# Optimization experiments

Measured on AMD Instinct MI355X. Metric: run time of the kernel, lower is better.

Reference implementation:

```python
import jax, jax.numpy as jnp
import numpy as np

N, E, D, NHID, NOUT, G = 100000, 600000, 128, 512, 768, 2048
EPS = 1e-5

def _lin_init(k, fi, fo):
    s = 1.0 / np.sqrt(fi)
    kw, kb = jax.random.split(k)
    W = jax.random.uniform(kw, (fi, fo), jnp.float32, -s, s)
    b = jax.random.uniform(kb, (fo,), jnp.float32, -s, s)
    return W, b

def setup_inputs():
    key = jax.random.key(0)
    ks = jax.random.split(key, 16)
    inp = {}
    inp['x'] = jax.random.normal(ks[0], (N, D), jnp.float32)
    inp['edge_index'] = jax.random.randint(ks[1], (2, E), 0, N, jnp.int32)
    inp['batch'] = jnp.sort(jax.random.randint(ks[2], (N,), 0, G, jnp.int32))
    # 3 GCN layers + GAT attention layer + 4 MLP linears
    inp['W1'], inp['b1'] = _lin_init(ks[3], D, D)
    inp['W2'], inp['b2'] = _lin_init(ks[4], D, D)
    inp['W3'], inp['b3'] = _lin_init(ks[5], D, D)
    inp['Wa'], inp['ba'] = _lin_init(ks[6], D, D)
    ka1, ka2 = jax.random.split(ks[7])
    inp['a_src'] = jax.random.normal(ka1, (D,), jnp.float32) * 0.1
    inp['a_dst'] = jax.random.normal(ka2, (D,), jnp.float32) * 0.1
    # batchnorm affine params (4 BNs)
    for i, nm in enumerate(['g1', 'g2', 'g3', 'ga']):
        inp[nm] = jnp.ones((D,), jnp.float32)
        inp['be' + nm[1:]] = jnp.zeros((D,), jnp.float32)
    inp['Wl1'], inp['bl1'] = _lin_init(ks[8], D, NHID)
    inp['Wl2'], inp['bl2'] = _lin_init(ks[9], NHID, NHID)
    inp['Wl3'], inp['bl3'] = _lin_init(ks[10], NHID, NHID)
    inp['Wl4'], inp['bl4'] = _lin_init(ks[11], NHID, NOUT)
    inp['gln'] = jnp.ones((NOUT,), jnp.float32)
    inp['bln'] = jnp.zeros((NOUT,), jnp.float32)
    return inp

def _bn(x, g, b):
    # training-mode batchnorm over node dim (biased variance, like torch)
    mu = jnp.mean(x, axis=0)
    var = jnp.var(x, axis=0)
    return (x - mu) * jax.lax.rsqrt(var + EPS) * g + b

def _forward(x, edge_index, batch, W1, b1, g1, be1, W2, b2, g2, be2, W3, b3, g3, be3,
             Wa, ba, a_src, a_dst, ga, bea, Wl1, bl1, Wl2, bl2, Wl3, bl3, Wl4, bl4, gln, bln):
    loop = jnp.arange(N, dtype=edge_index.dtype)
    src = jnp.concatenate([edge_index[0], loop])  # [E+N] with self-loops
    dst = jnp.concatenate([edge_index[1], loop])
    deg = jax.ops.segment_sum(jnp.ones_like(dst, jnp.float32), dst, num_segments=N)
    dinv = jax.lax.rsqrt(deg)  # deg >= 1 thanks to self-loops
    norm = (dinv[src] * dinv[dst])[:, None]  # [E+N, 1]

    def gcn(h, W, b):
        h = h @ W
        return jax.ops.segment_sum(h[src] * norm, dst, num_segments=N) + b

    x = jax.nn.relu(_bn(gcn(x, W1, b1), g1, be1)) + x
    x = jax.nn.relu(_bn(gcn(x, W2, b2), g2, be2)) + x
    x = jax.nn.relu(_bn(gcn(x, W3, b3), g3, be3)) + x

    # GATConv, heads=1: edge logit = LeakyReLU(a_src.h_j + a_dst.h_i), softmax over dst
    h = x @ Wa
    al = h @ a_src  # [N]
    ar = h @ a_dst
    e = jax.nn.leaky_relu(al[src] + ar[dst], 0.2)  # [E+N]
    m = jax.ops.segment_max(e, dst, num_segments=N)
    ee = jnp.exp(e - m[dst])
    denom = jax.ops.segment_sum(ee, dst, num_segments=N)
    alpha = (ee / denom[dst])[:, None]
    x = jax.ops.segment_sum(alpha * h[src], dst, num_segments=N) + ba
    x = jax.nn.relu(_bn(x, ga, bea))

    # global_add_pool
    x = jax.ops.segment_sum(x, batch, num_segments=G)  # [G, D]

    x = jax.nn.relu(x @ Wl1 + bl1)
    x = jax.nn.relu(x @ Wl2 + bl2)
    x = jax.nn.relu(x @ Wl3 + bl3)
    x = x @ Wl4 + bl4
    mu = jnp.mean(x, axis=-1, keepdims=True)
    var = jnp.var(x, axis=-1, keepdims=True)
    return (x - mu) * jax.lax.rsqrt(var + EPS) * gln + bln

def reference(x, edge_index, batch, W1, b1, g1, be1, W2, b2, g2, be2, W3, b3, g3, be3,
              Wa, ba, a_src, a_dst, ga, bea, Wl1, bl1, Wl2, bl2, Wl3, bl3, Wl4, bl4, gln, bln):
    return _forward(x, edge_index, batch, W1, b1, g1, be1, W2, b2, g2, be2, W3, b3, g3, be3,
                    Wa, ba, a_src, a_dst, ga, bea, Wl1, bl1, Wl2, bl2, Wl3, bl3, Wl4, bl4, gln, bln)
```

## Files before the change

kernel.cpp:

```cpp
#include <hip/hip_runtime.h>
#include <cstdint>
#include <cstddef>

#define CDIV(a,b) (((a)+(b)-1)/(b))

constexpr int N_ = 100000;
constexpr int E_ = 600000;
constexpr int D_ = 128;
constexpr int G_ = 2048;
constexpr int NHID_ = 512;
constexpr int NOUT_ = 768;
constexpr float EPS_ = 1e-5f;
constexpr int AGG_BLOCKS = 2048;

typedef short bf16x8 __attribute__((ext_vector_type(8)));
typedef float f32x4 __attribute__((ext_vector_type(4)));

__device__ __forceinline__ float wave_sum(float v){
#pragma unroll
  for (int m = 32; m; m >>= 1) v += __shfl_xor(v, m, 64);
  return v;
}
__device__ __forceinline__ float lrelu02(float v){ return v > 0.f ? v : 0.2f * v; }
__device__ __forceinline__ unsigned short f2bf(float f){
// ... 11 lines not shown
                     fmaxf(v.z*sc.z+sh.z, 0.f), fmaxf(v.w*sc.w+sh.w, 0.f));
}
__device__ __forceinline__ float4 add4(float4 a, float4 b){
  return make_float4(a.x+b.x, a.y+b.y, a.z+b.z, a.w+b.w);
}
__device__ __forceinline__ uint4 pk4(float4 lo, float4 hi){
  uint4 u;
  u.x = (unsigned)f2bf(lo.x) | ((unsigned)f2bf(hi.x) << 16);
  u.y = (unsigned)f2bf(lo.y) | ((unsigned)f2bf(hi.y) << 16);
  u.z = (unsigned)f2bf(lo.z) | ((unsigned)f2bf(hi.z) << 16);
  u.w = (unsigned)f2bf(lo.w) | ((unsigned)f2bf(hi.w) << 16);
  return u;
}
__device__ __forceinline__ bf16x8 mkaf(float4 lo, float4 hi){
  bf16x8 a;
  a[0]=(short)f2bf(lo.x); a[1]=(short)f2bf(lo.y); a[2]=(short)f2bf(lo.z); a[3]=(short)f2bf(lo.w);
  a[4]=(short)f2bf(hi.x); a[5]=(short)f2bf(hi.y); a[6]=(short)f2bf(hi.z); a[7]=(short)f2bf(hi.w);
  return a;
}
__device__ __forceinline__ bf16x8 mkaf_u(uint4 u){
  bf16x8 a;
  a[0]=(short)(u.x & 0xFFFF); a[4]=(short)(u.x >> 16);
  a[1]=(short)(u.y & 0xFFFF); a[5]=(short)(u.y >> 16);
  a[2]=(short)(u.z & 0xFFFF); a[6]=(short)(u.z >> 16);
  a[3]=(short)(u.w & 0xFFFF); a[7]=(short)(u.w >> 16);
  return a;
}

__global__ void k_count(const int* __restrict__ dst, int* __restrict__ cnt){
  int e = blockIdx.x * 256 + threadIdx.x;
  if (e < E_) atomicAdd(&cnt[dst[e]], 1);
}

__global__ void k_dinv(const int* __restrict__ cnt, float* __restrict__ dinv){
  int i = blockIdx.x * 256 + threadIdx.x;
  if (i < N_) dinv[i] = rsqrtf((float)(cnt[i] + 1));
}

__global__ void k_scan1(const int* __restrict__ cnt, int* __restrict__ ro, int* __restrict__ bs){
  __shared__ int s[256];
  int tid = threadIdx.x;
  int i = blockIdx.x * 256 + tid;
  int v = (i < N_) ? cnt[i] : 0;
  s[tid] = v; __syncthreads();
  for (int off = 1; off < 256; off <<= 1){
    int add = (tid >= off) ? s[tid - off] : 0;
    __syncthreads();
    s[tid] += add;
    __syncthreads();
  }
  if (i < N_) ro[i] = s[tid] - v;
  if (tid == 255) bs[blockIdx.x] = s[255];
}

__global__ void k_scan2(int* __restrict__ bs, int nb){
  __shared__ int s[512];
  int t = threadIdx.x;
  int v = (t < nb) ? bs[t] : 0;
  s[t] = v; __syncthreads();
  for (int off = 1; off < 512; off <<= 1){
    int a = (t >= off) ? s[t - off] : 0;
    __syncthreads();
    s[t] += a;
    __syncthreads();
  }
  if (t < nb) bs[t] = s[t] - v;
}

__global__ void k_scan3(int* __restrict__ ro, const int* __restrict__ bs){
  int i = blockIdx.x * 256 + threadIdx.x;
  if (i < N_) ro[i] += bs[i >> 8];
  if (i == N_) ro[N_] = E_;
}

__global__ void k_fill(const int* __restrict__ src, const int* __restrict__ dst,
                       const int* __restrict__ ro, int* __restrict__ cur, int* __restrict__ csr){
  int e = blockIdx.x * 256 + threadIdx.x;
  if (e < E_){
    int d = dst[e];
    int p = atomicAdd(&cur[d], 1);
    csr[ro[d] + p] = src[e];
  }
}

__global__ void k_bounds(const int* __restrict__ batch, int* __restrict__ gs){
  int g = blockIdx.x * 256 + threadIdx.x;
  if (g > G_) return;
  int lo = 0, hi = N_;
  while (lo < hi){ int mid = (lo + hi) >> 1; if (batch[mid] < g) lo = mid + 1; else hi = mid; }
  gs[g] = lo;
}

__global__ void k_wprep_g(const float* __restrict__ W, short* __restrict__ Wt, int K, int N){
  int i = blockIdx.x * 256 + threadIdx.x;
  int KT = K >> 5;
  int total = N * KT * 4;
  if (i >= total) return;
  int g = i & 3, t = (i >> 2) % KT, c = i / (KT * 4);
  short* o = Wt + (size_t)i * 8;
#pragma unroll
  for (int j = 0; j < 8; ++j){
    int k = t * 32 + (j >> 2) * 16 + g * 4 + (j & 3);
    o[j] = (short)f2bf(W[(size_t)k * N + c]);
  }
}

template<bool XB, bool RB>
__global__ __launch_bounds__(256) void k_mm_mfma(const void* __restrict__ Xin,
                                                 const short* __restrict__ Wt,
                                                 unsigned* __restrict__ hout,
                                                 const float* __restrict__ ss,
                                                 const void* __restrict__ resin,
                                                 unsigned* __restrict__ xnew,
                                                 const float* __restrict__ prescale,
                                                 const float* __restrict__ asrc,
                                                 const float* __restrict__ adst,
                                                 float* __restrict__ al_out,
                                                 float* __restrict__ ar_out){
  int lane = threadIdx.x & 63, wid = threadIdx.x >> 6;
  int cl = lane & 15, g = lane >> 4;
  int r0a = blockIdx.x * 128 + wid * 16;
  int r0b = r0a + 64;
  int rowa = r0a + cl, rowb = r0b + cl;
  bool va_ = rowa < N_, vb_ = rowb < N_;
  int rma = va_ ? rowa : 0;
  int rmb = vb_ ? rowb : 0;

  uint4 xua[4], xub[4];
  float4 xfa[8], xfb[8];
  uint4 rua[4], rub[4];
  float4 rfa[8], rfb[8];
  bool has_res = resin != nullptr;
  if (XB){
    const uint4* Xa = (const uint4*)((const unsigned*)Xin + (size_t)rma * 64);
    const uint4* Xb = (const uint4*)((const unsigned*)Xin + (size_t)rmb * 64);
#pragma unroll
    for (int t = 0; t < 4; ++t){ xua[t] = Xa[t*4 + g]; xub[t] = Xb[t*4 + g]; }
  } else {
    const float4* Xa = (const float4*)((const float*)Xin + (size_t)rma * 128);
    const float4* Xb = (const float4*)((const float*)Xin + (size_t)rmb * 128);
#pragma unroll
    for (int t = 0; t < 4; ++t){
      xfa[2*t] = Xa[t*8 + g]; xfa[2*t+1] = Xa[t*8 + g + 4];
      xfb[2*t] = Xb[t*8 + g]; xfb[2*t+1] = Xb[t*8 + g + 4];
    }
  }
  if (has_res){
    if (RB){
      const uint4* Ra = (const uint4*)((const unsigned*)resin + (size_t)rma * 64);
      const uint4* Rb = (const uint4*)((const unsigned*)resin + (size_t)rmb * 64);
#pragma unroll
      for (int t = 0; t < 4; ++t){ rua[t] = Ra[t*4 + g]; rub[t] = Rb[t*4 + g]; }
    } else {
      const float4* Ra = (const float4*)((const float*)resin + (size_t)rma * 128);
      const float4* Rb = (const float4*)((const float*)resin + (size_t)rmb * 128);
#pragma unroll
      for (int t = 0; t < 4; ++t){
        rfa[2*t] = Ra[t*8 + g]; rfa[2*t+1] = Ra[t*8 + g + 4];
        rfb[2*t] = Rb[t*8 + g]; rfb[2*t+1] = Rb[t*8 + g + 4];
      }
    }
  }
  __builtin_amdgcn_sched_barrier(0);

  bf16x8 afa[4], afb[4];
#pragma unroll
  for (int t = 0; t < 4; ++t){
    float4 la, ha, lb, hb;
    if (XB){
      la = unplo(xua[t]); ha = unphi(xua[t]);
      lb = unplo(xub[t]); hb = unphi(xub[t]);
    } else {
      la = xfa[2*t]; ha = xfa[2*t+1];
      lb = xfb[2*t]; hb = xfb[2*t+1];
    }
    if (ss){
      int f0 = t * 32 + g * 4;
      float4 sc0 = *(const float4*)&ss[f0],      sh0 = *(const float4*)&ss[128 + f0];
      float4 sc1 = *(const float4*)&ss[f0 + 16], sh1 = *(const float4*)&ss[128 + f0 + 16];
      la = bnrelu4(la, sc0, sh0); ha = bnrelu4(ha, sc1, sh1);
      lb = bnrelu4(lb, sc0, sh0); hb = bnrelu4(hb, sc1, sh1);
      if (has_res){
        if (RB){
          la = add4(la, unplo(rua[t])); ha = add4(ha, unphi(rua[t]));
          lb = add4(lb, unplo(rub[t])); hb = add4(hb, unphi(rub[t]));
        } else {
          la = add4(la, rfa[2*t]); ha = add4(ha, rfa[2*t+1]);
          lb = add4(lb, rfb[2*t]); hb = add4(hb, rfb[2*t+1]);
        }
      }
      if (xnew){
        if (va_) *(uint4*)(xnew + (size_t)rowa * 64 + t*16 + g*4) = pk4(la, ha);
        if (vb_) *(uint4*)(xnew + (size_t)rowb * 64 + t*16 + g*4) = pk4(lb, hb);
      }
    }
    afa[t] = mkaf(la, ha);
    afb[t] = mkaf(lb, hb);
  }

  f32x4 accA[8], accB[8];
#pragma unroll
  for (int j = 0; j < 8; ++j){ accA[j] = (f32x4){0,0,0,0}; accB[j] = (f32x4){0,0,0,0}; }
#pragma unroll
  for (int t = 0; t < 4; ++t){
#pragma unroll
    for (int j = 0; j < 8; ++j){
      int c = j * 16 + cl;
      bf16x8 bf = *(const bf16x8*)(Wt + ((size_t)c * 16 + t * 4 + g) * 8);
      accA[j] = __builtin_amdgcn_mfma_f32_16x16x32_bf16(afa[t], bf, accA[j], 0, 0, 0);
      accB[j] = __builtin_amdgcn_mfma_f32_16x16x32_bf16(afb[t], bf, accB[j], 0, 0, 0);
    }
  }

#pragma unroll
  for (int r = 0; r < 4; ++r){
    int ra = r0a + g * 4 + r;
    if (ra < N_){
      float psc = prescale ? prescale[ra] : 1.f;
#pragma unroll
      for (int jp = 0; jp < 4; ++jp){
        unsigned lo = f2bf(accA[2*jp][r] * psc);
        unsigned hi = f2bf(accA[2*jp+1][r] * psc);
        hout[(size_t)ra * 64 + jp * 16 + cl] = (hi << 16) | lo;
      }
    }
    int rb = r0b + g * 4 + r;
    if (rb < N_){
      float psc = prescale ? prescale[rb] : 1.f;
#pragma unroll
      for (int jp = 0; jp < 4; ++jp){
        unsigned lo = f2bf(accB[2*jp][r] * psc);
        unsigned hi = f2bf(accB[2*jp+1][r] * psc);
        hout[(size_t)rb * 64 + jp * 16 + cl] = (hi << 16) | lo;
      }
    }
  }

  if (al_out){
    float pal[8] = {0,0,0,0,0,0,0,0}, par[8] = {0,0,0,0,0,0,0,0};
#pragma unroll
    for (int j = 0; j < 8; ++j){
      float as_ = asrc[j * 16 + cl], ad_ = adst[j * 16 + cl];
#pragma unroll
      for (int r = 0; r < 4; ++r){
        pal[r]   += accA[j][r] * as_; par[r]   += accA[j][r] * ad_;
        pal[4+r] += accB[j][r] * as_; par[4+r] += accB[j][r] * ad_;
      }
    }
#pragma unroll
    for (int m = 1; m < 16; m <<= 1)
#pragma unroll
      for (int r = 0; r < 8; ++r){
        pal[r] += __shfl_xor(pal[r], m, 64);
        par[r] += __shfl_xor(par[r], m, 64);
      }
    if (cl == 0){
#pragma unroll
      for (int r = 0; r < 4; ++r){
        int ra = r0a + g * 4 + r;
        if (ra < N_){ al_out[ra] = pal[r]; ar_out[ra] = par[r]; }
        int rb = r0b + g * 4 + r;
        if (rb < N_){ al_out[rb] = pal[4+r]; ar_out[rb] = par[4+r]; }
      }
    }
  }
}

__global__ __launch_bounds__(256) void k_gcn_agg2(const unsigned* __restrict__ hbf, const int* __restrict__ ro,
                          const int* __restrict__ csr, const float* __restrict__ dinv,
                          const float* __restrict__ bias, unsigned* __restrict__ outb,
                          float4* __restrict__ pbuf){
  int wid = threadIdx.x >> 6, lane = threadIdx.x & 63;
  int f0 = 32 * (lane >> 4) + (lane & 15), f1 = f0 + 16;
  float bb0 = bias[f0], bb1 = bias[f1];
  float S0 = 0.f, S1 = 0.f, Q0 = 0.f, Q1 = 0.f;
  for (int node = blockIdx.x * 4 + wid; node < N_; node += AGG_BLOCKS * 4){
    int s0 = ro[node], s1 = ro[node + 1];
    int deg = s1 - s0;
    float di = dinv[node];
    unsigned us = hbf[(size_t)node * 64 + lane];
    float a0 = bflo(us), a1 = bfhi(us);
    if (deg <= 64){
      int sidx = (lane < deg) ? csr[s0 + lane] : 0;
      int j = 0;
      for (; j + 4 <= deg; j += 4){
        int sa = __shfl(sidx, j, 64),   sb = __shfl(sidx, j+1, 64);
        int sc = __shfl(sidx, j+2, 64), sd = __shfl(sidx, j+3, 64);
        unsigned ua = hbf[(size_t)sa*64+lane], ub = hbf[(size_t)sb*64+lane];
        unsigned uc = hbf[(size_t)sc*64+lane], ud = hbf[(size_t)sd*64+lane];
        a0 += bflo(ua) + bflo(ub) + bflo(uc) + bflo(ud);
        a1 += bfhi(ua) + bfhi(ub) + bfhi(uc) + bfhi(ud);
      }
      for (; j < deg; ++j){
        int s = __shfl(sidx, j, 64);
        unsigned u = hbf[(size_t)s*64+lane];
        a0 += bflo(u); a1 += bfhi(u);
      }
    } else {
      for (int base = s0; base < s1; base += 64){
        int c = min(64, s1 - base);
        int sidx = (lane < c) ? csr[base + lane] : 0;
        for (int j = 0; j < c; ++j){
          int s = __shfl(sidx, j, 64);
          unsigned u = hbf[(size_t)s*64+lane];
          a0 += bflo(u); a1 += bfhi(u);
        }
      }
    }
    float o0 = di * a0 + bb0;
    float o1 = di * a1 + bb1;
    outb[(size_t)node * 64 + lane] = (unsigned)f2bf(o0) | ((unsigned)f2bf(o1) << 16);
    S0 += o0; S1 += o1; Q0 += o0*o0; Q1 += o1*o1;
  }
  __shared__ float4 sred[4][64];
  sred[wid][lane] = make_float4(S0, S1, Q0, Q1);
  __syncthreads();
  if (wid == 0){
    float4 t = sred[0][lane];
    float4 u1 = sred[1][lane], u2 = sred[2][lane], u3 = sred[3][lane];
    t.x += u1.x + u2.x + u3.x;
    t.y += u1.y + u2.y + u3.y;
    t.z += u1.z + u2.z + u3.z;
    t.w += u1.w + u2.w + u3.w;
    pbuf[(size_t)blockIdx.x * 64 + lane] = t;
  }
}

__global__ __launch_bounds__(256) void k_gat_agg2(const unsigned* __restrict__ hbf, const int* __restrict__ ro,
                          const int* __restrict__ csr, const float* __restrict__ al,
                          const float* __restrict__ ar, const float* __restrict__ bias,
                          unsigned* __restrict__ outb, float4* __restrict__ pbuf){
  int wid = threadIdx.x >> 6, lane = threadIdx.x & 63;
  int f0 = 32 * (lane >> 4) + (lane & 15), f1 = f0 + 16;
  float bb0 = bias[f0], bb1 = bias[f1];
  float S0 = 0.f, S1 = 0.f, Q0 = 0.f, Q1 = 0.f;
  for (int node = blockIdx.x * 4 + wid; node < N_; node += AGG_BLOCKS * 4){
    int s0 = ro[node], s1 = ro[node + 1];
    int deg = s1 - s0;
    float ari = ar[node], ali = al[node];
    float pself = __expf(lrelu02(ali + ari));
    unsigned uself = hbf[(size_t)node * 64 + lane];
    float h0 = bflo(uself), h1 = bfhi(uself);
    float a0, a1;
    if (deg <= 64){
      int sidx = 0; float p = 0.f;
      if (lane < deg){ sidx = csr[s0 + lane]; p = __expf(lrelu02(al[sidx] + ari)); }
      float invd = 1.f / (wave_sum(p) + pself);
      float wl = p * invd;
      float wsf = pself * invd;
      a0 = wsf * h0; a1 = wsf * h1;
      int j = 0;
      for (; j + 4 <= deg; j += 4){
        int sa = __shfl(sidx, j, 64),   sb = __shfl(sidx, j+1, 64);
        int sc = __shfl(sidx, j+2, 64), sd = __shfl(sidx, j+3, 64);
        float wa = __shfl(wl, j, 64),   wb = __shfl(wl, j+1, 64);
        float wc = __shfl(wl, j+2, 64), wd = __shfl(wl, j+3, 64);
        unsigned ua = hbf[(size_t)sa*64+lane], ub = hbf[(size_t)sb*64+lane];
        unsigned uc = hbf[(size_t)sc*64+lane], ud = hbf[(size_t)sd*64+lane];
        a0 += wa*bflo(ua) + wb*bflo(ub) + wc*bflo(uc) + wd*bflo(ud);
        a1 += wa*bfhi(ua) + wb*bfhi(ub) + wc*bfhi(uc) + wd*bfhi(ud);
      }
      for (; j < deg; ++j){
        int s = __shfl(sidx, j, 64); float w = __shfl(wl, j, 64);
        unsigned u = hbf[(size_t)s*64+lane];
// ... 5 lines not shown
        int c = min(64, s1 - base);
        float p = 0.f;
        if (lane < c) p = __expf(lrelu02(al[csr[base + lane]] + ari));
        denom += wave_sum(p);
      }
      float invd = 1.f / denom;
      float wsf = pself * invd;
      a0 = wsf * h0; a1 = wsf * h1;
      for (int base = s0; base < s1; base += 64){
        int c = min(64, s1 - base);
        int sidx = 0; float wl = 0.f;
        if (lane < c){ sidx = csr[base + lane]; wl = __expf(lrelu02(al[sidx] + ari)) * invd; }
        for (int j = 0; j < c; ++j){
          int s = __shfl(sidx, j, 64); float w = __shfl(wl, j, 64);
          unsigned u = hbf[(size_t)s*64+lane];
          a0 += w*bflo(u); a1 += w*bfhi(u);
        }
      }
    }
    float o0 = a0 + bb0, o1 = a1 + bb1;
    outb[(size_t)node * 64 + lane] = (unsigned)f2bf(o0) | ((unsigned)f2bf(o1) << 16);
    S0 += o0; S1 += o1; Q0 += o0*o0; Q1 += o1*o1;
  }
  __shared__ float4 sred[4][64];
  sred[wid][lane] = make_float4(S0, S1, Q0, Q1);
  __syncthreads();
  if (wid == 0){
    float4 t = sred[0][lane];
    float4 u1 = sred[1][lane], u2 = sred[2][lane], u3 = sred[3][lane];
    t.x += u1.x + u2.x + u3.x;
    t.y += u1.y + u2.y + u3.y;
    t.z += u1.z + u2.z + u3.z;
    t.w += u1.w + u2.w + u3.w;
    pbuf[(size_t)blockIdx.x * 64 + lane] = t;
  }
}

__global__ void k_bn_reduce(const float4* __restrict__ pbuf, const float* __restrict__ g,
                            const float* __restrict__ be, float* __restrict__ ss){
  int c = blockIdx.x;
  int f0 = 32 * (c >> 4) + (c & 15), f1 = f0 + 16;
  float4 a = make_float4(0.f, 0.f, 0.f, 0.f);
  for (int r = threadIdx.x; r < AGG_BLOCKS; r += 256){
    float4 v = pbuf[(size_t)r * 64 + c];
    a.x += v.x; a.y += v.y; a.z += v.z; a.w += v.w;
  }
  __shared__ float4 s[256];
  s[threadIdx.x] = a; __syncthreads();
  for (int off = 128; off; off >>= 1){
    if (threadIdx.x < off){
      float4 o = s[threadIdx.x + off];
      s[threadIdx.x].x += o.x; s[threadIdx.x].y += o.y;
      s[threadIdx.x].z += o.z; s[threadIdx.x].w += o.w;
    }
    __syncthreads();
  }
  if (threadIdx.x == 0){
    float4 t = s[0];
    float inv_n = 1.f / (float)N_;
    float mean0 = t.x * inv_n, mean1 = t.y * inv_n;
    float var0 = fmaxf(t.z * inv_n - mean0 * mean0, 0.f);
    float var1 = fmaxf(t.w * inv_n - mean1 * mean1, 0.f);
    float sc0 = g[f0] * rsqrtf(var0 + EPS_);
    float sc1 = g[f1] * rsqrtf(var1 + EPS_);
    ss[f0] = sc0; ss[f1] = sc1;
    ss[128 + f0] = be[f0] - mean0 * sc0;
    ss[128 + f1] = be[f1] - mean1 * sc1;
  }
}

__global__ void k_pool2(const unsigned* __restrict__ xn, const int* __restrict__ gs,
                        const float* __restrict__ ss, unsigned* __restrict__ pooled){
  int g = blockIdx.x, f = threadIdx.x & 127, half = threadIdx.x >> 7;
  int idx = ((f >> 5) << 4) | (f & 15);
  int hi = (f >> 4) & 1;
  int s = gs[g], e = gs[g + 1];
  float sc = ss[f], sh = ss[128 + f];
  float a = 0.f;
  for (int n = s + half; n < e; n += 2){
    unsigned u = xn[(size_t)n * 64 + idx];
    float v = hi ? bfhi(u) : bflo(u);
    a += fmaxf(v * sc + sh, 0.f);
  }
  __shared__ float red[256];
  red[threadIdx.x] = a; __syncthreads();
  if (half == 0 && hi == 0){
    float vlo = red[f] + red[f + 128];
    float vhi = red[f + 16] + red[f + 16 + 128];
    pooled[(size_t)g * 64 + idx] = (unsigned)f2bf(vlo) | ((unsigned)f2bf(vhi) << 16);
  }
}

template<int K, bool RELU, bool OUTF32>
__global__ __launch_bounds__(256) void k_gemm_mfma(const unsigned* __restrict__ A,
                                                   const short* __restrict__ Wt,
                                                   const float* __restrict__ bias,
                                                   void* __restrict__ Cout, int Ncols){
  constexpr int KT = K >> 5;
  int lane = threadIdx.x & 63, wid = threadIdx.x >> 6;
  int cl = lane & 15, g = lane >> 4;
  int row0 = blockIdx.y * 64 + wid * 16;
  int cb = blockIdx.x;
  int arow = row0 + cl;
  const uint4* Ar = (const uint4*)(A + (size_t)arow * (K / 2));

  f32x4 acc[8];
#pragma unroll
  for (int j = 0; j < 8; ++j) acc[j] = (f32x4){0,0,0,0};

  for (int t = 0; t < KT; ++t){
// ... 74 lines not shown
  const int*   batch = (const int*)d_in[2];
  const float* W1 = (const float*)d_in[3];  const float* b1 = (const float*)d_in[4];
  const float* W2 = (const float*)d_in[5];  const float* b2 = (const float*)d_in[6];
  const float* W3 = (const float*)d_in[7];  const float* b3 = (const float*)d_in[8];
  const float* Wa = (const float*)d_in[9];  const float* ba = (const float*)d_in[10];
  const float* a_src = (const float*)d_in[11]; const float* a_dst = (const float*)d_in[12];
  const float* g1 = (const float*)d_in[13]; const float* be1 = (const float*)d_in[14];
  const float* g2 = (const float*)d_in[15]; const float* be2 = (const float*)d_in[16];
  const float* g3 = (const float*)d_in[17]; const float* be3 = (const float*)d_in[18];
  const float* ga = (const float*)d_in[19]; const float* bea = (const float*)d_in[20];
  const float* Wl1 = (const float*)d_in[21]; const float* bl1 = (const float*)d_in[22];
  const float* Wl2 = (const float*)d_in[23]; const float* bl2 = (const float*)d_in[24];
  const float* Wl3 = (const float*)d_in[25]; const float* bl3 = (const float*)d_in[26];
  const float* Wl4 = (const float*)d_in[27]; const float* bl4 = (const float*)d_in[28];
  const float* gln = (const float*)d_in[29]; const float* bln = (const float*)d_in[30];
  float* out = (float*)d_out;

  char* base = (char*)d_ws;
  size_t off = 0;
  auto alloc = [&](size_t bytes)->char*{
    char* p = base + off;
    off += (bytes + 255) & ~(size_t)255;
    return p;
  };
  int*   cnt    = (int*)  alloc((size_t)N_ * 4);
  float* dinv   = (float*)alloc((size_t)N_ * 4);
  int*   ro     = (int*)  alloc((size_t)(N_ + 1) * 4);
  int*   bs     = (int*)  alloc(512 * 4);
  int*   cur    = (int*)  alloc((size_t)N_ * 4);
  int*   csr    = (int*)  alloc((size_t)E_ * 4);
  int*   gstart = (int*)  alloc((size_t)(G_ + 1) * 4);
  float* al     = (float*)alloc((size_t)N_ * 4);
  float* ar     = (float*)alloc((size_t)N_ * 4);
  float* ss     = (float*)alloc(256 * 4);
  float4* pbuf  = (float4*)alloc((size_t)AGG_BLOCKS * 64 * 16);
  short* wt1    = (short*)alloc((size_t)128 * 128 * 2);
  short* wt2    = (short*)alloc((size_t)128 * 128 * 2);
  short* wt3    = (short*)alloc((size_t)128 * 128 * 2);
  short* wta    = (short*)alloc((size_t)128 * 128 * 2);
  short* wtl1   = (short*)alloc((size_t)128 * NHID_ * 2);
  short* wtl2   = (short*)alloc((size_t)NHID_ * NHID_ * 2);
  short* wtl3   = (short*)alloc((size_t)NHID_ * NHID_ * 2);
  short* wtl4   = (short*)alloc((size_t)NHID_ * NOUT_ * 2);
  unsigned* bufH  = (unsigned*)alloc((size_t)N_ * 64 * 4);
  unsigned* bufYb = (unsigned*)alloc((size_t)N_ * 64 * 4);
  unsigned* xresb = (unsigned*)alloc((size_t)N_ * 64 * 4);
  unsigned* pooled= (unsigned*)alloc((size_t)G_ * 64 * 4);
  unsigned* m1b   = (unsigned*)alloc((size_t)G_ * (NHID_/2) * 4);
  unsigned* m2b   = (unsigned*)alloc((size_t)G_ * (NHID_/2) * 4);
  float* m4     = (float*)alloc((size_t)G_ * NOUT_ * 4);
  (void)ws_size; (void)in_sizes; (void)n_in; (void)out_size;

  const int nbE = CDIV(E_, 256), nbN = CDIV(N_, 256);
  const int MMB = CDIV(N_, 128);

  hipMemsetAsync(cnt, 0, (size_t)N_ * 4, stream);
  k_count<<<nbE, 256, 0, stream>>>(dst, cnt);
  k_dinv<<<nbN, 256, 0, stream>>>(cnt, dinv);
  k_scan1<<<nbN, 256, 0, stream>>>(cnt, ro, bs);
  k_scan2<<<1, 512, 0, stream>>>(bs, nbN);
  k_scan3<<<CDIV(N_ + 1, 256), 256, 0, stream>>>(ro, bs);
  hipMemsetAsync(cur, 0, (size_t)N_ * 4, stream);
  k_fill<<<nbE, 256, 0, stream>>>(src, dst, ro, cur, csr);
  k_bounds<<<CDIV(G_ + 1, 256), 256, 0, stream>>>(batch, gstart);
  k_wprep_g<<<8, 256, 0, stream>>>(W1, wt1, 128, 128);
  k_wprep_g<<<8, 256, 0, stream>>>(W2, wt2, 128, 128);
  k_wprep_g<<<8, 256, 0, stream>>>(W3, wt3, 128, 128);
  k_wprep_g<<<8, 256, 0, stream>>>(Wa, wta, 128, 128);
  k_wprep_g<<<CDIV(NHID_*4*4, 256), 256, 0, stream>>>(Wl1, wtl1, 128, NHID_);
  k_wprep_g<<<CDIV(NHID_*16*4, 256), 256, 0, stream>>>(Wl2, wtl2, NHID_, NHID_);
  k_wprep_g<<<CDIV(NHID_*16*4, 256), 256, 0, stream>>>(Wl3, wtl3, NHID_, NHID_);
  k_wprep_g<<<CDIV(NOUT_*16*4, 256), 256, 0, stream>>>(Wl4, wtl4, NHID_, NOUT_);

  k_mm_mfma<false,false><<<MMB, 256, 0, stream>>>(x, wt1, bufH, nullptr, nullptr, nullptr,
                                                  dinv, nullptr, nullptr, nullptr, nullptr);
  k_gcn_agg2<<<AGG_BLOCKS, 256, 0, stream>>>(bufH, ro, csr, dinv, b1, bufYb, pbuf);
  k_bn_reduce<<<64, 256, 0, stream>>>(pbuf, g1, be1, ss);
  k_mm_mfma<true,false><<<MMB, 256, 0, stream>>>(bufYb, wt2, bufH, ss, x, xresb,
                                                 dinv, nullptr, nullptr, nullptr, nullptr);
  k_gcn_agg2<<<AGG_BLOCKS, 256, 0, stream>>>(bufH, ro, csr, dinv, b2, bufYb, pbuf);
  k_bn_reduce<<<64, 256, 0, stream>>>(pbuf, g2, be2, ss);
  k_mm_mfma<true,true><<<MMB, 256, 0, stream>>>(bufYb, wt3, bufH, ss, xresb, xresb,
                                                dinv, nullptr, nullptr, nullptr, nullptr);
  k_gcn_agg2<<<AGG_BLOCKS, 256, 0, stream>>>(bufH, ro, csr, dinv, b3, bufYb, pbuf);
  k_bn_reduce<<<64, 256, 0, stream>>>(pbuf, g3, be3, ss);
  k_mm_mfma<true,true><<<MMB, 256, 0, stream>>>(bufYb, wta, bufH, ss, xresb, nullptr,
                                                nullptr, a_src, a_dst, al, ar);
  k_gat_agg2<<<AGG_BLOCKS, 256, 0, stream>>>(bufH, ro, csr, al, ar, ba, bufYb, pbuf);
  k_bn_reduce<<<64, 256, 0, stream>>>(pbuf, ga, bea, ss);
  k_pool2<<<G_, 256, 0, stream>>>(bufYb, gstart, ss, pooled);
  k_gemm_mfma<128, true, false><<<dim3(NHID_/128, G_/64), 256, 0, stream>>>(pooled, wtl1, bl1, m1b, NHID_);
  k_gemm_mfma<512, true, false><<<dim3(NHID_/128, G_/64), 256, 0, stream>>>(m1b, wtl2, bl2, m2b, NHID_);
  k_gemm_mfma<512, true, false><<<dim3(NHID_/128, G_/64), 256, 0, stream>>>(m2b, wtl3, bl3, m1b, NHID_);
  k_gemm_mfma<512, false, true><<<dim3(NOUT_/128, G_/64), 256, 0, stream>>>(m1b, wtl4, bl4, m4, NOUT_);
  k_layernorm<<<G_, 256, 0, stream>>>(m4, gln, bln, out);
}
```

Measured before the change: 550.6 us.

## Fuse dinv into scan, batch weight prep into one launch, halve matmul row tile

Computes dinv inside the first scan kernel, removing a separate launch and a re-read of the counts. The eight weight-prep launches become one kernel that finds its matrix from an offsets table. The node matmul now gives each block 64 rows and each wave one 16-row tile instead of two, doubling the grid and cutting register pressure. In exchange, each B fragment loaded from the weights feeds only one MFMA instead of two.

```diff
diff --git a/kernel.cpp b/kernel.cpp
--- a/kernel.cpp
+++ b/kernel.cpp
@@ -67,12 +67,8 @@
   if (e < E_) atomicAdd(&cnt[dst[e]], 1);
 }
 
-__global__ void k_dinv(const int* __restrict__ cnt, float* __restrict__ dinv){
-  int i = blockIdx.x * 256 + threadIdx.x;
-  if (i < N_) dinv[i] = rsqrtf((float)(cnt[i] + 1));
-}
-
-__global__ void k_scan1(const int* __restrict__ cnt, int* __restrict__ ro, int* __restrict__ bs){
+__global__ void k_scan1(const int* __restrict__ cnt, int* __restrict__ ro, int* __restrict__ bs,
+                        float* __restrict__ dinv){
   __shared__ int s[256];
   int tid = threadIdx.x;
   int i = blockIdx.x * 256 + tid;
@@ -84,7 +80,10 @@
     s[tid] += add;
     __syncthreads();
   }
-  if (i < N_) ro[i] = s[tid] - v;
+  if (i < N_){
+    ro[i] = s[tid] - v;
+    dinv[i] = rsqrtf((float)(v + 1));
+  }
   if (tid == 255) bs[blockIdx.x] = s[255];
 }
 
@@ -126,17 +125,29 @@
   gs[g] = lo;
 }
 
-__global__ void k_wprep_g(const float* __restrict__ W, short* __restrict__ Wt, int K, int N){
+struct WprepArgs {
+  const float* W[8];
+  short* Wt[8];
+  int K[8];
+  int N[8];
+  int ofs[9];
+};
+
+__global__ void k_wprep_all(WprepArgs a){
   int i = blockIdx.x * 256 + threadIdx.x;
+  if (i >= a.ofs[8]) return;
+  int m = 0;
+  while (i >= a.ofs[m + 1]) ++m;
+  int li = i - a.ofs[m];
+  int K = a.K[m], Nn = a.N[m];
   int KT = K >> 5;
-  int total = N * KT * 4;
-  if (i >= total) return;
-  int g = i & 3, t = (i >> 2) % KT, c = i / (KT * 4);
-  short* o = Wt + (size_t)i * 8;
+  int g = li & 3, t = (li >> 2) % KT, c = li / (KT * 4);
+  short* o = a.Wt[m] + (size_t)li * 8;
+  const float* W = a.W[m];
 #pragma unroll
   for (int j = 0; j < 8; ++j){
     int k = t * 32 + (j >> 2) * 16 + g * 4 + (j & 3);
-    o[j] = (short)f2bf(W[(size_t)k * N + c]);
+    o[j] = (short)f2bf(W[(size_t)k * Nn + c]);
   }
 }
 
@@ -154,148 +165,103 @@
                                                  float* __restrict__ ar_out){
   int lane = threadIdx.x & 63, wid = threadIdx.x >> 6;
   int cl = lane & 15, g = lane >> 4;
-  int r0a = blockIdx.x * 128 + wid * 16;
-  int r0b = r0a + 64;
-  int rowa = r0a + cl, rowb = r0b + cl;
-  bool va_ = rowa < N_, vb_ = rowb < N_;
-  int rma = va_ ? rowa : 0;
-  int rmb = vb_ ? rowb : 0;
-
-  uint4 xua[4], xub[4];
-  float4 xfa[8], xfb[8];
-  uint4 rua[4], rub[4];
-  float4 rfa[8], rfb[8];
+  int rw0 = blockIdx.x * 64 + wid * 16;
+  int arow = rw0 + cl;
+  bool rv = arow < N_;
+  int rm = rv ? arow : 0;
   bool has_res = resin != nullptr;
+
+  uint4 xu[4]; float4 xf[8];
+  uint4 ru[4]; float4 rf[8];
   if (XB){
-    const uint4* Xa = (const uint4*)((const unsigned*)Xin + (size_t)rma * 64);
-    const uint4* Xb = (const uint4*)((const unsigned*)Xin + (size_t)rmb * 64);
-#pragma unroll
-    for (int t = 0; t < 4; ++t){ xua[t] = Xa[t*4 + g]; xub[t] = Xb[t*4 + g]; }
+    const uint4* Xr = (const uint4*)((const unsigned*)Xin + (size_t)rm * 64);
+#pragma unroll
+    for (int t = 0; t < 4; ++t) xu[t] = Xr[t*4 + g];
   } else {
-    const float4* Xa = (const float4*)((const float*)Xin + (size_t)rma * 128);
-    const float4* Xb = (const float4*)((const float*)Xin + (size_t)rmb * 128);
-#pragma unroll
-    for (int t = 0; t < 4; ++t){
-      xfa[2*t] = Xa[t*8 + g]; xfa[2*t+1] = Xa[t*8 + g + 4];
-      xfb[2*t] = Xb[t*8 + g]; xfb[2*t+1] = Xb[t*8 + g + 4];
-    }
+    const float4* Xr = (const float4*)((const float*)Xin + (size_t)rm * 128);
+#pragma unroll
+    for (int t = 0; t < 4; ++t){ xf[2*t] = Xr[t*8 + g]; xf[2*t+1] = Xr[t*8 + g + 4]; }
   }
   if (has_res){
     if (RB){
-      const uint4* Ra = (const uint4*)((const unsigned*)resin + (size_t)rma * 64);
-      const uint4* Rb = (const uint4*)((const unsigned*)resin + (size_t)rmb * 64);
-#pragma unroll
-      for (int t = 0; t < 4; ++t){ rua[t] = Ra[t*4 + g]; rub[t] = Rb[t*4 + g]; }
+      const uint4* Rr = (const uint4*)((const unsigned*)resin + (size_t)rm * 64);
+#pragma unroll
+      for (int t = 0; t < 4; ++t) ru[t] = Rr[t*4 + g];
     } else {
-      const float4* Ra = (const float4*)((const float*)resin + (size_t)rma * 128);
-      const float4* Rb = (const float4*)((const float*)resin + (size_t)rmb * 128);
-#pragma unroll
-      for (int t = 0; t < 4; ++t){
-        rfa[2*t] = Ra[t*8 + g]; rfa[2*t+1] = Ra[t*8 + g + 4];
-        rfb[2*t] = Rb[t*8 + g]; rfb[2*t+1] = Rb[t*8 + g + 4];
-      }
+      const float4* Rr = (const float4*)((const float*)resin + (size_t)rm * 128);
+#pragma unroll
+      for (int t = 0; t < 4; ++t){ rf[2*t] = Rr[t*8 + g]; rf[2*t+1] = Rr[t*8 + g + 4]; }
     }
   }
   __builtin_amdgcn_sched_barrier(0);
 
-  bf16x8 afa[4], afb[4];
+  bf16x8 af[4];
 #pragma unroll
   for (int t = 0; t < 4; ++t){
-    float4 la, ha, lb, hb;
-    if (XB){
-      la = unplo(xua[t]); ha = unphi(xua[t]);
-      lb = unplo(xub[t]); hb = unphi(xub[t]);
-    } else {
-      la = xfa[2*t]; ha = xfa[2*t+1];
-      lb = xfb[2*t]; hb = xfb[2*t+1];
-    }
+    float4 lo, hi;
+    if (XB){ lo = unplo(xu[t]); hi = unphi(xu[t]); }
+    else    { lo = xf[2*t];     hi = xf[2*t+1];    }
     if (ss){
       int f0 = t * 32 + g * 4;
       float4 sc0 = *(const float4*)&ss[f0],      sh0 = *(const float4*)&ss[128 + f0];
       float4 sc1 = *(const float4*)&ss[f0 + 16], sh1 = *(const float4*)&ss[128 + f0 + 16];
-      la = bnrelu4(la, sc0, sh0); ha = bnrelu4(ha, sc1, sh1);
-      lb = bnrelu4(lb, sc0, sh0); hb = bnrelu4(hb, sc1, sh1);
+      lo = bnrelu4(lo, sc0, sh0); hi = bnrelu4(hi, sc1, sh1);
       if (has_res){
-        if (RB){
-          la = add4(la, unplo(rua[t])); ha = add4(ha, unphi(rua[t]));
-          lb = add4(lb, unplo(rub[t])); hb = add4(hb, unphi(rub[t]));
-        } else {
-          la = add4(la, rfa[2*t]); ha = add4(ha, rfa[2*t+1]);
-          lb = add4(lb, rfb[2*t]); hb = add4(hb, rfb[2*t+1]);
-        }
-      }
-      if (xnew){
-        if (va_) *(uint4*)(xnew + (size_t)rowa * 64 + t*16 + g*4) = pk4(la, ha);
-        if (vb_) *(uint4*)(xnew + (size_t)rowb * 64 + t*16 + g*4) = pk4(lb, hb);
-      }
-    }
-    afa[t] = mkaf(la, ha);
-    afb[t] = mkaf(lb, hb);
-  }
-
-  f32x4 accA[8], accB[8];
-#pragma unroll
-  for (int j = 0; j < 8; ++j){ accA[j] = (f32x4){0,0,0,0}; accB[j] = (f32x4){0,0,0,0}; }
+        if (RB){ lo = add4(lo, unplo(ru[t])); hi = add4(hi, unphi(ru[t])); }
+        else    { lo = add4(lo, rf[2*t]);     hi = add4(hi, rf[2*t+1]);    }
+      }
+      if (xnew && rv) *(uint4*)(xnew + (size_t)arow * 64 + t*16 + g*4) = pk4(lo, hi);
+    }
+    af[t] = mkaf(lo, hi);
+  }
+
+  f32x4 acc[8];
+#pragma unroll
+  for (int j = 0; j < 8; ++j) acc[j] = (f32x4){0,0,0,0};
 #pragma unroll
   for (int t = 0; t < 4; ++t){
 #pragma unroll
     for (int j = 0; j < 8; ++j){
       int c = j * 16 + cl;
       bf16x8 bf = *(const bf16x8*)(Wt + ((size_t)c * 16 + t * 4 + g) * 8);
-      accA[j] = __builtin_amdgcn_mfma_f32_16x16x32_bf16(afa[t], bf, accA[j], 0, 0, 0);
-      accB[j] = __builtin_amdgcn_mfma_f32_16x16x32_bf16(afb[t], bf, accB[j], 0, 0, 0);
+      acc[j] = __builtin_amdgcn_mfma_f32_16x16x32_bf16(af[t], bf, acc[j], 0, 0, 0);
     }
   }
 
 #pragma unroll
   for (int r = 0; r < 4; ++r){
-    int ra = r0a + g * 4 + r;
-    if (ra < N_){
-      float psc = prescale ? prescale[ra] : 1.f;
+    int row = rw0 + g * 4 + r;
+    if (row < N_){
+      float psc = prescale ? prescale[row] : 1.f;
 #pragma unroll
       for (int jp = 0; jp < 4; ++jp){
-        unsigned lo = f2bf(accA[2*jp][r] * psc);
-        unsigned hi = f2bf(accA[2*jp+1][r] * psc);
-        hout[(size_t)ra * 64 + jp * 16 + cl] = (hi << 16) | lo;
-      }
-    }
-    int rb = r0b + g * 4 + r;
-    if (rb < N_){
-      float psc = prescale ? prescale[rb] : 1.f;
-#pragma unroll
-      for (int jp = 0; jp < 4; ++jp){
-        unsigned lo = f2bf(accB[2*jp][r] * psc);
-        unsigned hi = f2bf(accB[2*jp+1][r] * psc);
-        hout[(size_t)rb * 64 + jp * 16 + cl] = (hi << 16) | lo;
+        unsigned lo = f2bf(acc[2*jp][r] * psc);
+        unsigned hi = f2bf(acc[2*jp+1][r] * psc);
+        hout[(size_t)row * 64 + jp * 16 + cl] = (hi << 16) | lo;
       }
     }
   }
 
   if (al_out){
-    float pal[8] = {0,0,0,0,0,0,0,0}, par[8] = {0,0,0,0,0,0,0,0};
+    float pal[4] = {0,0,0,0}, par[4] = {0,0,0,0};
 #pragma unroll
     for (int j = 0; j < 8; ++j){
       float as_ = asrc[j * 16 + cl], ad_ = adst[j * 16 + cl];
 #pragma unroll
+      for (int r = 0; r < 4; ++r){ pal[r] += acc[j][r] * as_; par[r] += acc[j][r] * ad_; }
+    }
+#pragma unroll
+    for (int m = 1; m < 16; m <<= 1)
+#pragma unroll
       for (int r = 0; r < 4; ++r){
-        pal[r]   += accA[j][r] * as_; par[r]   += accA[j][r] * ad_;
-        pal[4+r] += accB[j][r] * as_; par[4+r] += accB[j][r] * ad_;
-      }
-    }
-#pragma unroll
-    for (int m = 1; m < 16; m <<= 1)
-#pragma unroll
-      for (int r = 0; r < 8; ++r){
         pal[r] += __shfl_xor(pal[r], m, 64);
         par[r] += __shfl_xor(par[r], m, 64);
       }
     if (cl == 0){
 #pragma unroll
       for (int r = 0; r < 4; ++r){
-        int ra = r0a + g * 4 + r;
-        if (ra < N_){ al_out[ra] = pal[r]; ar_out[ra] = par[r]; }
-        int rb = r0b + g * 4 + r;
-        if (rb < N_){ al_out[rb] = pal[4+r]; ar_out[rb] = par[4+r]; }
+        int row = rw0 + g * 4 + r;
+        if (row < N_){ al_out[row] = pal[r]; ar_out[row] = par[r]; }
       }
     }
   }
@@ -640,25 +606,32 @@
   (void)ws_size; (void)in_sizes; (void)n_in; (void)out_size;
 
   const int nbE = CDIV(E_, 256), nbN = CDIV(N_, 256);
-  const int MMB = CDIV(N_, 128);
+  const int MMB = CDIV(N_, 64);
 
   hipMemsetAsync(cnt, 0, (size_t)N_ * 4, stream);
   k_count<<<nbE, 256, 0, stream>>>(dst, cnt);
-  k_dinv<<<nbN, 256, 0, stream>>>(cnt, dinv);
-  k_scan1<<<nbN, 256, 0, stream>>>(cnt, ro, bs);
+  k_scan1<<<nbN, 256, 0, stream>>>(cnt, ro, bs, dinv);
   k_scan2<<<1, 512, 0, stream>>>(bs, nbN);
   k_scan3<<<CDIV(N_ + 1, 256), 256, 0, stream>>>(ro, bs);
   hipMemsetAsync(cur, 0, (size_t)N_ * 4, stream);
   k_fill<<<nbE, 256, 0, stream>>>(src, dst, ro, cur, csr);
   k_bounds<<<CDIV(G_ + 1, 256), 256, 0, stream>>>(batch, gstart);
-  k_wprep_g<<<8, 256, 0, stream>>>(W1, wt1, 128, 128);
-  k_wprep_g<<<8, 256, 0, stream>>>(W2, wt2, 128, 128);
-  k_wprep_g<<<8, 256, 0, stream>>>(W3, wt3, 128, 128);
-  k_wprep_g<<<8, 256, 0, stream>>>(Wa, wta, 128, 128);
-  k_wprep_g<<<CDIV(NHID_*4*4, 256), 256, 0, stream>>>(Wl1, wtl1, 128, NHID_);
-  k_wprep_g<<<CDIV(NHID_*16*4, 256), 256, 0, stream>>>(Wl2, wtl2, NHID_, NHID_);
-  k_wprep_g<<<CDIV(NHID_*16*4, 256), 256, 0, stream>>>(Wl3, wtl3, NHID_, NHID_);
-  k_wprep_g<<<CDIV(NOUT_*16*4, 256), 256, 0, stream>>>(Wl4, wtl4, NHID_, NOUT_);
+
+  {
+    WprepArgs a;
+    const float* Ws[8] = {W1, W2, W3, Wa, Wl1, Wl2, Wl3, Wl4};
+    short* Wts[8] = {wt1, wt2, wt3, wta, wtl1, wtl2, wtl3, wtl4};
+    int Ks[8] = {128,128,128,128, 128, NHID_, NHID_, NHID_};
+    int Ns[8] = {128,128,128,128, NHID_, NHID_, NHID_, NOUT_};
+    int run = 0;
+    for (int m = 0; m < 8; ++m){
+      a.W[m] = Ws[m]; a.Wt[m] = Wts[m]; a.K[m] = Ks[m]; a.N[m] = Ns[m];
+      a.ofs[m] = run;
+      run += Ns[m] * (Ks[m] >> 5) * 4;
+    }
+    a.ofs[8] = run;
+    k_wprep_all<<<CDIV(run, 256), 256, 0, stream>>>(a);
+  }
 
   k_mm_mfma<false,false><<<MMB, 256, 0, stream>>>(x, wt1, bufH, nullptr, nullptr, nullptr,
                                                   dinv, nullptr, nullptr, nullptr, nullptr);
```

Measured after the change: 547.6 us. No clear change (-0.6%).

## Cut kernel launches by fusing BN reduce, dinv and weight prep

Applied to the files above, without the earlier changes.

Removes the separate batchnorm-reduce kernels by having the aggregation kernels atomically accumulate per-feature sums into a small zeroed buffer, and each consumer kernel derives scale and shift itself in shared memory. Folds the dinv computation into the scan kernel and merges eight weight-prep launches into one kernel driven by an offset table. The goal is fewer launches and less serialization on the stream. In exchange it adds float atomics, which introduce contention and make the summation order nondeterministic, and every matmul block repeats the small BN-parameter computation.

```diff
diff --git a/kernel.cpp b/kernel.cpp
--- a/kernel.cpp
+++ b/kernel.cpp
@@ -67,12 +67,8 @@
   if (e < E_) atomicAdd(&cnt[dst[e]], 1);
 }
 
-__global__ void k_dinv(const int* __restrict__ cnt, float* __restrict__ dinv){
-  int i = blockIdx.x * 256 + threadIdx.x;
-  if (i < N_) dinv[i] = rsqrtf((float)(cnt[i] + 1));
-}
-
-__global__ void k_scan1(const int* __restrict__ cnt, int* __restrict__ ro, int* __restrict__ bs){
+__global__ void k_scan1(const int* __restrict__ cnt, int* __restrict__ ro, int* __restrict__ bs,
+                        float* __restrict__ dinv){
   __shared__ int s[256];
   int tid = threadIdx.x;
   int i = blockIdx.x * 256 + tid;
@@ -84,7 +80,10 @@
     s[tid] += add;
     __syncthreads();
   }
-  if (i < N_) ro[i] = s[tid] - v;
+  if (i < N_){
+    ro[i] = s[tid] - v;
+    dinv[i] = rsqrtf((float)(v + 1));
+  }
   if (tid == 255) bs[blockIdx.x] = s[255];
 }
 
@@ -109,7 +108,14 @@
 }
 
 __global__ void k_fill(const int* __restrict__ src, const int* __restrict__ dst,
-                       const int* __restrict__ ro, int* __restrict__ cur, int* __restrict__ csr){
+                       const int* __restrict__ ro, int* __restrict__ cur, int* __restrict__ csr,
+                       float* __restrict__ bnz){
+  if (blockIdx.x == 0){
+    bnz[threadIdx.x] = 0.f;
+    bnz[threadIdx.x + 256] = 0.f;
+    bnz[threadIdx.x + 512] = 0.f;
+    bnz[threadIdx.x + 768] = 0.f;
+  }
   int e = blockIdx.x * 256 + threadIdx.x;
   if (e < E_){
     int d = dst[e];
@@ -126,17 +132,29 @@
   gs[g] = lo;
 }
 
-__global__ void k_wprep_g(const float* __restrict__ W, short* __restrict__ Wt, int K, int N){
+struct WprepArgs {
+  const float* W[8];
+  short* Wt[8];
+  int K[8];
+  int N[8];
+  int ofs[9];
+};
+
+__global__ void k_wprep_all(WprepArgs a){
   int i = blockIdx.x * 256 + threadIdx.x;
+  if (i >= a.ofs[8]) return;
+  int m = 0;
+  while (i >= a.ofs[m + 1]) ++m;
+  int li = i - a.ofs[m];
+  int K = a.K[m], Nn = a.N[m];
   int KT = K >> 5;
-  int total = N * KT * 4;
-  if (i >= total) return;
-  int g = i & 3, t = (i >> 2) % KT, c = i / (KT * 4);
-  short* o = Wt + (size_t)i * 8;
+  int g = li & 3, t = (li >> 2) % KT, c = li / (KT * 4);
+  short* o = a.Wt[m] + (size_t)li * 8;
+  const float* W = a.W[m];
 #pragma unroll
   for (int j = 0; j < 8; ++j){
     int k = t * 32 + (j >> 2) * 16 + g * 4 + (j & 3);
-    o[j] = (short)f2bf(W[(size_t)k * N + c]);
+    o[j] = (short)f2bf(W[(size_t)k * Nn + c]);
   }
 }
 
@@ -144,7 +162,9 @@
 __global__ __launch_bounds__(256) void k_mm_mfma(const void* __restrict__ Xin,
                                                  const short* __restrict__ Wt,
                                                  unsigned* __restrict__ hout,
-                                                 const float* __restrict__ ss,
+                                                 const float* __restrict__ bnsum,
+                                                 const float* __restrict__ gam,
+                                                 const float* __restrict__ bet,
                                                  const void* __restrict__ resin,
                                                  unsigned* __restrict__ xnew,
                                                  const float* __restrict__ prescale,
@@ -152,6 +172,7 @@
                                                  const float* __restrict__ adst,
                                                  float* __restrict__ al_out,
                                                  float* __restrict__ ar_out){
+  __shared__ float lss[256];
   int lane = threadIdx.x & 63, wid = threadIdx.x >> 6;
   int cl = lane & 15, g = lane >> 4;
   int r0a = blockIdx.x * 128 + wid * 16;
@@ -160,12 +181,13 @@
   bool va_ = rowa < N_, vb_ = rowb < N_;
   int rma = va_ ? rowa : 0;
   int rmb = vb_ ? rowb : 0;
+  bool has_res = resin != nullptr;
+  bool has_bn = bnsum != nullptr;
 
   uint4 xua[4], xub[4];
   float4 xfa[8], xfb[8];
   uint4 rua[4], rub[4];
   float4 rfa[8], rfb[8];
-  bool has_res = resin != nullptr;
   if (XB){
     const uint4* Xa = (const uint4*)((const unsigned*)Xin + (size_t)rma * 64);
     const uint4* Xb = (const uint4*)((const unsigned*)Xin + (size_t)rmb * 64);
@@ -195,6 +217,19 @@
         rfb[2*t] = Rb[t*8 + g]; rfb[2*t+1] = Rb[t*8 + g + 4];
       }
     }
+  }
+
+  if (has_bn){
+    int t = threadIdx.x;
+    if (t < 128){
+      float inv_n = 1.f / (float)N_;
+      float mean = bnsum[t] * inv_n;
+      float var = fmaxf(bnsum[128 + t] * inv_n - mean * mean, 0.f);
+      float sc = gam[t] * rsqrtf(var + EPS_);
+      lss[t] = sc;
+      lss[128 + t] = bet[t] - mean * sc;
+    }
+    __syncthreads();
   }
   __builtin_amdgcn_sched_barrier(0);
 
@@ -209,10 +244,10 @@
       la = xfa[2*t]; ha = xfa[2*t+1];
       lb = xfb[2*t]; hb = xfb[2*t+1];
     }
-    if (ss){
+    if (has_bn){
       int f0 = t * 32 + g * 4;
-      float4 sc0 = *(const float4*)&ss[f0],      sh0 = *(const float4*)&ss[128 + f0];
-      float4 sc1 = *(const float4*)&ss[f0 + 16], sh1 = *(const float4*)&ss[128 + f0 + 16];
+      float4 sc0 = *(const float4*)&lss[f0],      sh0 = *(const float4*)&lss[128 + f0];
+      float4 sc1 = *(const float4*)&lss[f0 + 16], sh1 = *(const float4*)&lss[128 + f0 + 16];
       la = bnrelu4(la, sc0, sh0); ha = bnrelu4(ha, sc1, sh1);
       lb = bnrelu4(lb, sc0, sh0); hb = bnrelu4(hb, sc1, sh1);
       if (has_res){
@@ -304,7 +339,7 @@
 __global__ __launch_bounds__(256) void k_gcn_agg2(const unsigned* __restrict__ hbf, const int* __restrict__ ro,
                           const int* __restrict__ csr, const float* __restrict__ dinv,
                           const float* __restrict__ bias, unsigned* __restrict__ outb,
-                          float4* __restrict__ pbuf){
+                          float* __restrict__ bnsum){
   int wid = threadIdx.x >> 6, lane = threadIdx.x & 63;
   int f0 = 32 * (lane >> 4) + (lane & 15), f1 = f0 + 16;
   float bb0 = bias[f0], bb1 = bias[f1];
@@ -357,14 +392,17 @@
     t.y += u1.y + u2.y + u3.y;
     t.z += u1.z + u2.z + u3.z;
     t.w += u1.w + u2.w + u3.w;
-    pbuf[(size_t)blockIdx.x * 64 + lane] = t;
+    atomicAdd(&bnsum[f0], t.x);
+    atomicAdd(&bnsum[f1], t.y);
+    atomicAdd(&bnsum[128 + f0], t.z);
+    atomicAdd(&bnsum[128 + f1], t.w);
   }
 }
 
 __global__ __launch_bounds__(256) void k_gat_agg2(const unsigned* __restrict__ hbf, const int* __restrict__ ro,
                           const int* __restrict__ csr, const float* __restrict__ al,
                           const float* __restrict__ ar, const float* __restrict__ bias,
-                          unsigned* __restrict__ outb, float4* __restrict__ pbuf){
+                          unsigned* __restrict__ outb, float* __restrict__ bnsum){
   int wid = threadIdx.x >> 6, lane = threadIdx.x & 63;
   int f0 = 32 * (lane >> 4) + (lane & 15), f1 = f0 + 16;
   float bb0 = bias[f0], bb1 = bias[f1];
@@ -436,50 +474,34 @@
     t.y += u1.y + u2.y + u3.y;
     t.z += u1.z + u2.z + u3.z;
     t.w += u1.w + u2.w + u3.w;
-    pbuf[(size_t)blockIdx.x * 64 + lane] = t;
-  }
-}
-
-__global__ void k_bn_reduce(const float4* __restrict__ pbuf, const float* __restrict__ g,
-                            const float* __restrict__ be, float* __restrict__ ss){
-  int c = blockIdx.x;
-  int f0 = 32 * (c >> 4) + (c & 15), f1 = f0 + 16;
-  float4 a = make_float4(0.f, 0.f, 0.f, 0.f);
-  for (int r = threadIdx.x; r < AGG_BLOCKS; r += 256){
-    float4 v = pbuf[(size_t)r * 64 + c];
-    a.x += v.x; a.y += v.y; a.z += v.z; a.w += v.w;
-  }
-  __shared__ float4 s[256];
-  s[threadIdx.x] = a; __syncthreads();
-  for (int off = 128; off; off >>= 1){
-    if (threadIdx.x < off){
-      float4 o = s[threadIdx.x + off];
-      s[threadIdx.x].x += o.x; s[threadIdx.x].y += o.y;
-      s[threadIdx.x].z += o.z; s[threadIdx.x].w += o.w;
-    }
-    __syncthreads();
-  }
-  if (threadIdx.x == 0){
-    float4 t = s[0];
-    float inv_n = 1.f / (float)N_;
-    float mean0 = t.x * inv_n, mean1 = t.y * inv_n;
-    float var0 = fmaxf(t.z * inv_n - mean0 * mean0, 0.f);
-    float var1 = fmaxf(t.w * inv_n - mean1 * mean1, 0.f);
-    float sc0 = g[f0] * rsqrtf(var0 + EPS_);
-    float sc1 = g[f1] * rsqrtf(var1 + EPS_);
-    ss[f0] = sc0; ss[f1] = sc1;
-    ss[128 + f0] = be[f0] - mean0 * sc0;
-    ss[128 + f1] = be[f1] - mean1 * sc1;
+    atomicAdd(&bnsum[f0], t.x);
+    atomicAdd(&bnsum[f1], t.y);
+    atomicAdd(&bnsum[128 + f0], t.z);
+    atomicAdd(&bnsum[128 + f1], t.w);
   }
 }
 
 __global__ void k_pool2(const unsigned* __restrict__ xn, const int* __restrict__ gs,
-                        const float* __restrict__ ss, unsigned* __restrict__ pooled){
+                        const float* __restrict__ bnsum, const float* __restrict__ gam,
+                        const float* __restrict__ bet, unsigned* __restrict__ pooled){
+  __shared__ float lss[256];
+  {
+    int t = threadIdx.x;
+    if (t < 128){
+      float inv_n = 1.f / (float)N_;
+      float mean = bnsum[t] * inv_n;
+      float var = fmaxf(bnsum[128 + t] * inv_n - mean * mean, 0.f);
+      float sc = gam[t] * rsqrtf(var + EPS_);
+      lss[t] = sc;
+      lss[128 + t] = bet[t] - mean * sc;
+    }
+  }
+  __syncthreads();
   int g = blockIdx.x, f = threadIdx.x & 127, half = threadIdx.x >> 7;
   int idx = ((f >> 5) << 4) | (f & 15);
   int hi = (f >> 4) & 1;
   int s = gs[g], e = gs[g + 1];
-  float sc = ss[f], sh = ss[128 + f];
+  float sc = lss[f], sh = lss[128 + f];
   float a = 0.f;
   for (int n = s + half; n < e; n += 2){
     unsigned u = xn[(size_t)n * 64 + idx];
@@ -620,8 +642,7 @@
   int*   gstart = (int*)  alloc((size_t)(G_ + 1) * 4);
   float* al     = (float*)alloc((size_t)N_ * 4);
   float* ar     = (float*)alloc((size_t)N_ * 4);
-  float* ss     = (float*)alloc(256 * 4);
-  float4* pbuf  = (float4*)alloc((size_t)AGG_BLOCKS * 64 * 16);
+  float* bnsum  = (float*)alloc(1024 * 4);
   short* wt1    = (short*)alloc((size_t)128 * 128 * 2);
   short* wt2    = (short*)alloc((size_t)128 * 128 * 2);
   short* wt3    = (short*)alloc((size_t)128 * 128 * 2);
@@ -639,44 +660,52 @@
   float* m4     = (float*)alloc((size_t)G_ * NOUT_ * 4);
   (void)ws_size; (void)in_sizes; (void)n_in; (void)out_size;
 
+  float* bn0 = bnsum;
+  float* bn1 = bnsum + 256;
+  float* bn2 = bnsum + 512;
+  float* bn3 = bnsum + 768;
+
   const int nbE = CDIV(E_, 256), nbN = CDIV(N_, 256);
   const int MMB = CDIV(N_, 128);
 
   hipMemsetAsync(cnt, 0, (size_t)N_ * 4, stream);
   k_count<<<nbE, 256, 0, stream>>>(dst, cnt);
-  k_dinv<<<nbN, 256, 0, stream>>>(cnt, dinv);
-  k_scan1<<<nbN, 256, 0, stream>>>(cnt, ro, bs);
+  k_scan1<<<nbN, 256, 0, stream>>>(cnt, ro, bs, dinv);
   k_scan2<<<1, 512, 0, stream>>>(bs, nbN);
   k_scan3<<<CDIV(N_ + 1, 256), 256, 0, stream>>>(ro, bs);
   hipMemsetAsync(cur, 0, (size_t)N_ * 4, stream);
-  k_fill<<<nbE, 256, 0, stream>>>(src, dst, ro, cur, csr);
+  k_fill<<<nbE, 256, 0, stream>>>(src, dst, ro, cur, csr, bnsum);
   k_bounds<<<CDIV(G_ + 1, 256), 256, 0, stream>>>(batch, gstart);
-  k_wprep_g<<<8, 256, 0, stream>>>(W1, wt1, 128, 128);
-  k_wprep_g<<<8, 256, 0, stream>>>(W2, wt2, 128, 128);
-  k_wprep_g<<<8, 256, 0, stream>>>(W3, wt3, 128, 128);
-  k_wprep_g<<<8, 256, 0, stream>>>(Wa, wta, 128, 128);
-  k_wprep_g<<<CDIV(NHID_*4*4, 256), 256, 0, stream>>>(Wl1, wtl1, 128, NHID_);
-  k_wprep_g<<<CDIV(NHID_*16*4, 256), 256, 0, stream>>>(Wl2, wtl2, NHID_, NHID_);
-  k_wprep_g<<<CDIV(NHID_*16*4, 256), 256, 0, stream>>>(Wl3, wtl3, NHID_, NHID_);
-  k_wprep_g<<<CDIV(NOUT_*16*4, 256), 256, 0, stream>>>(Wl4, wtl4, NHID_, NOUT_);
+
+  {
+    WprepArgs a;
+    const float* Ws[8] = {W1, W2, W3, Wa, Wl1, Wl2, Wl3, Wl4};
+    short* Wts[8] = {wt1, wt2, wt3, wta, wtl1, wtl2, wtl3, wtl4};
+    int Ks[8] = {128,128,128,128, 128, NHID_, NHID_, NHID_};
+    int Ns[8] = {128,128,128,128, NHID_, NHID_, NHID_, NOUT_};
+    int run = 0;
+    for (int m = 0; m < 8; ++m){
+      a.W[m] = Ws[m]; a.Wt[m] = Wts[m]; a.K[m] = Ks[m]; a.N[m] = Ns[m];
+      a.ofs[m] = run;
+      run += Ns[m] * (Ks[m] >> 5) * 4;
+    }
+    a.ofs[8] = run;
+    k_wprep_all<<<CDIV(run, 256), 256, 0, stream>>>(a);
+  }
 
   k_mm_mfma<false,false><<<MMB, 256, 0, stream>>>(x, wt1, bufH, nullptr, nullptr, nullptr,
-                                                  dinv, nullptr, nullptr, nullptr, nullptr);
-  k_gcn_agg2<<<AGG_BLOCKS, 256, 0, stream>>>(bufH, ro, csr, dinv, b1, bufYb, pbuf);
-  k_bn_reduce<<<64, 256, 0, stream>>>(pbuf, g1, be1, ss);
-  k_mm_mfma<true,false><<<MMB, 256, 0, stream>>>(bufYb, wt2, bufH, ss, x, xresb,
-                                                 dinv, nullptr, nullptr, nullptr, nullptr);
-  k_gcn_agg2<<<AGG_BLOCKS, 256, 0, stream>>>(bufH, ro, csr, dinv, b2, bufYb, pbuf);
-  k_bn_reduce<<<64, 256, 0, stream>>>(pbuf, g2, be2, ss);
-  k_mm_mfma<true,true><<<MMB, 256, 0, stream>>>(bufYb, wt3, bufH, ss, xresb, xresb,
-                                                dinv, nullptr, nullptr, nullptr, nullptr);
-  k_gcn_agg2<<<AGG_BLOCKS, 256, 0, stream>>>(bufH, ro, csr, dinv, b3, bufYb, pbuf);
-  k_bn_reduce<<<64, 256, 0, stream>>>(pbuf, g3, be3, ss);
-  k_mm_mfma<true,true><<<MMB, 256, 0, stream>>>(bufYb, wta, bufH, ss, xresb, nullptr,
-                                                nullptr, a_src, a_dst, al, ar);
-  k_gat_agg2<<<AGG_BLOCKS, 256, 0, stream>>>(bufH, ro, csr, al, ar, ba, bufYb, pbuf);
-  k_bn_reduce<<<64, 256, 0, stream>>>(pbuf, ga, bea, ss);
-  k_pool2<<<G_, 256, 0, stream>>>(bufYb, gstart, ss, pooled);
+                                                  nullptr, nullptr, dinv, nullptr, nullptr, nullptr, nullptr);
+  k_gcn_agg2<<<AGG_BLOCKS, 256, 0, stream>>>(bufH, ro, csr, dinv, b1, bufYb, bn0);
+  k_mm_mfma<true,false><<<MMB, 256, 0, stream>>>(bufYb, wt2, bufH, bn0, g1, be1,
+                                                 x, xresb, dinv, nullptr, nullptr, nullptr, nullptr);
+  k_gcn_agg2<<<AGG_BLOCKS, 256, 0, stream>>>(bufH, ro, csr, dinv, b2, bufYb, bn1);
+  k_mm_mfma<true,true><<<MMB, 256, 0, stream>>>(bufYb, wt3, bufH, bn1, g2, be2,
+                                                xresb, xresb, dinv, nullptr, nullptr, nullptr, nullptr);
+  k_gcn_agg2<<<AGG_BLOCKS, 256, 0, stream>>>(bufH, ro, csr, dinv, b3, bufYb, bn2);
+  k_mm_mfma<true,true><<<MMB, 256, 0, stream>>>(bufYb, wta, bufH, bn2, g3, be3,
+                                                xresb, nullptr, nullptr, a_src, a_dst, al, ar);
+  k_gat_agg2<<<AGG_BLOCKS, 256, 0, stream>>>(bufH, ro, csr, al, ar, ba, bufYb, bn3);
+  k_pool2<<<G_, 256, 0, stream>>>(bufYb, gstart, bn3, ga, bea, pooled);
   k_gemm_mfma<128, true, false><<<dim3(NHID_/128, G_/64), 256, 0, stream>>>(pooled, wtl1, bl1, m1b, NHID_);
   k_gemm_mfma<512, true, false><<<dim3(NHID_/128, G_/64), 256, 0, stream>>>(m1b, wtl2, bl2, m2b, NHID_);
   k_gemm_mfma<512, true, false><<<dim3(NHID_/128, G_/64), 256, 0, stream>>>(m2b, wtl3, bl3, m1b, NHID_);
```

Result: slower. 670.0 us (+21.7%).
